# Performance work log

Measured on AMD Instinct MI355X. Metric: run time of the kernel, lower is better.

Reference implementation:

```python
import jax, jax.numpy as jnp
import numpy as np
from jax import lax

B, H, W = 2, 960, 1280
K = 1024            # max_keypoints
P = 256             # num_pairs (BAD descriptor dim)
NUM_SCALES = 3
DIFF_ITERS = 3
KAPPA = 0.05
TAU = 0.2           # explicit FED step size (stable < 0.25)
DET_THRESHOLD = 0.001
AKAZE_NMS = 5       # detector-internal NMS window
NMS_WIN = 2 * 3 + 1 # pipeline NMS window (nms_radius=3)
ORI_PATCH = 15
ORI_SIGMA = 2.5
SINK_ITERS = 20
EPSILON = 1.0
UNUSED_SCORE = 1.0
MAX_RADIUS = 5

def _conv(x, k):
    return lax.conv_general_dilated(x, k, (1, 1), 'SAME', dimension_numbers=('NCHW', 'OIHW', 'NCHW'))

_sob = np.array([[-1., 0., 1.], [-2., 0., 2.], [-1., 0., 1.]], np.float32) / 8.0
KX = jnp.asarray(_sob)[None, None]
KY = jnp.asarray(_sob.T)[None, None]
_d2 = np.array([[0., 0., 0.], [1., -2., 1.], [0., 0., 0.]], np.float32)
KXX = jnp.asarray(_d2)[None, None]
KYY = jnp.asarray(_d2.T)[None, None]

# Gaussian weighting kernel for orientation estimation
_c = np.arange(ORI_PATCH, dtype=np.float32) - (ORI_PATCH - 1) / 2.0
_gy, _gx = np.meshgrid(_c, _c, indexing='ij')
_g = np.exp(-(_gx ** 2 + _gy ** 2) / (2.0 * ORI_SIGMA ** 2))
GK = jnp.asarray((_g / _g.sum()).astype(np.float32))[None, None]

# Box-average kernel bank: one normalized box filter per radius 0..MAX_RADIUS
_bc = np.arange(-MAX_RADIUS, MAX_RADIUS + 1, dtype=np.float32)
_by, _bx = np.meshgrid(_bc, _bc, indexing='ij')
_rv = np.arange(MAX_RADIUS + 1, dtype=np.float32)[:, None, None]
_bm = ((np.abs(_by) <= _rv) & (np.abs(_bx) <= _rv)).astype(np.float32)
BOX_BANK = jnp.asarray((_bm / (2.0 * _rv + 1.0) ** 2)[:, None])  # [R+1,1,11,11]

def _shifts(a):
    p = jnp.pad(a, ((0, 0), (0, 0), (1, 1), (1, 1)), mode='edge')
    return p[:, :, :-2, 1:-1], p[:, :, 2:, 1:-1], p[:, :, 1:-1, :-2], p[:, :, 1:-1, 2:]

def _fed_step(L):
    # One explicit Perona-Malik (FED) nonlinear diffusion step
    Lx = _conv(L, KX); Ly = _conv(L, KY)
    g = 1.0 / (1.0 + (Lx * Lx + Ly * Ly) / (KAPPA * KAPPA))
    Ln, Ls, Lw, Le = _shifts(L)
    gn, gs, gw, ge = _shifts(g)
    flux = 0.5 * ((g + gn) * (Ln - L) + (g + gs) * (Ls - L) + (g + gw) * (Lw - L) + (g + ge) * (Le - L))
    return L + TAU * flux

def _maxpool(s, win):
    return lax.reduce_window(s, -jnp.inf, lax.max, (1, win, win), (1, 1, 1), 'SAME')

def _akaze(img):
    # Multi-scale FED diffusion -> Hessian determinant response + orientation map
    L = img
    resp = jnp.zeros((B, H, W), img.dtype)
    for _s in range(NUM_SCALES):
        for _i in range(DIFF_ITERS):
            L = _fed_step(L)
        Lxx = _conv(L, KXX); Lyy = _conv(L, KYY); Lxy = _conv(_conv(L, KX), KY)
        resp = jnp.maximum(resp, (Lxx * Lyy - Lxy * Lxy)[:, 0])
    resp = jnp.where(resp > DET_THRESHOLD, resp, 0.0)
    resp = resp * (resp >= _maxpool(resp, AKAZE_NMS) - 1e-7).astype(resp.dtype)
    gxs = _conv(_conv(img, KX), GK)[:, 0]
    gys = _conv(_conv(img, KY), GK)[:, 0]
    theta = jnp.arctan2(gys, gxs)  # [B,H,W]
    return resp, theta

def _select(resp):
    # Pipeline-level maxpool NMS + top-K selection, pad invalid with (-1,-1)
    mask = (resp >= _maxpool(resp, NMS_WIN) - 1e-7).astype(resp.dtype)
    s = resp * mask
    s = jnp.where(s > 0.0, s, 0.0)
    tk, idx = lax.top_k(s.reshape(B, -1), K)
    y = (idx // W).astype(jnp.float32)
    x = (idx % W).astype(jnp.float32)
    valid = (tk > 0.0).astype(jnp.float32)
    kpts = jnp.where(valid[..., None] > 0.5, jnp.stack([y, x], -1), -1.0)
    return kpts, tk * valid, valid

def _bad(img, kpts, theta, valid, offsets, radii, thresholds):
    # Orientation-aware BAD: box-averaged intensity differences at rotated pair offsets
    bank = _conv(img, BOX_BANK)  # [B,R+1,H,W]
    yc = jnp.clip(kpts[..., 0], 0.0, H - 1.0)
    xc = jnp.clip(kpts[..., 1], 0.0, W - 1.0)
    yi = jnp.round(yc).astype(jnp.int32); xi = jnp.round(xc).astype(jnp.int32)
    th = jax.vmap(lambda m, a, b: m[a, b])(theta, yi, xi)  # [B,K] nearest-sampled orientation
    c = jnp.cos(th)[..., None]; s = jnp.sin(th)[..., None]
    ox1, oy1, ox2, oy2 = offsets[:, 0], offsets[:, 1], offsets[:, 2], offsets[:, 3]
    px1 = xc[..., None] + c * ox1 - s * oy1
    py1 = yc[..., None] + s * ox1 + c * oy1
    px2 = xc[..., None] + c * ox2 - s * oy2
    py2 = yc[..., None] + s * ox2 + c * oy2
    rb = jnp.broadcast_to(radii[None, :], (K, P))
    def samp(px, py):
        xi_ = jnp.clip(jnp.round(px), 0, W - 1).astype(jnp.int32)
        yi_ = jnp.clip(jnp.round(py), 0, H - 1).astype(jnp.int32)
        return jax.vmap(lambda bk, a, b: bk[rb, a, b])(bank, yi_, xi_)  # [B,K,P]
    v = (samp(px1, py1) - samp(px2, py2)) - thresholds[None, None, :]
    v = v * valid[..., None]
    n = jnp.linalg.norm(v, axis=-1, keepdims=True)
    return v / (n + 1e-8)

def _sinkhorn(d1, d2):
    sq1 = jnp.sum(d1 * d1, -1); sq2 = jnp.sum(d2 * d2, -1)
    dist2 = sq1[:, :, None] + sq2[:, None, :] - 2.0 * jnp.einsum('bip,bjp->bij', d1, d2)
    dist = jnp.sqrt(jnp.maximum(dist2, 0.0) + 1e-12)
    Z = jnp.full((B, K + 1, K + 1), UNUSED_SCORE, d1.dtype)
    Z = Z.at[:, :K, :K].set(-dist) / EPSILON
    norm = -jnp.log(2.0 * K)
    log_mu = jnp.concatenate([jnp.zeros(K, Z.dtype), jnp.log(float(K)) * jnp.ones(1, Z.dtype)]) + norm
    log_nu = log_mu
    def body(carry, _):
        u, v = carry
        u = log_mu[None] - jax.nn.logsumexp(Z + v[:, None, :], axis=2)
        v = log_nu[None] - jax.nn.logsumexp(Z + u[:, :, None], axis=1)
        return (u, v), None
    (u, v), _ = lax.scan(body, (jnp.zeros((B, K + 1), Z.dtype), jnp.zeros((B, K + 1), Z.dtype)), None, length=SINK_ITERS)
    return jnp.exp(Z + u[:, :, None] + v[:, None, :] - norm)  # [B,K+1,K+1]

def _forward(img1, img2, offsets, thresholds, radii):
    r1, t1 = _akaze(img1)
    r2, t2 = _akaze(img2)
    k1, s1, v1 = _select(r1)
    k2, s2, v2 = _select(r2)
    d1 = _bad(img1, k1, t1, v1, offsets, radii, thresholds)
    d2 = _bad(img2, k2, t2, v2, offsets, radii, thresholds)
    probs = _sinkhorn(d1, d2)
    return k1, k2, probs

def setup_inputs():
    key = jax.random.key(0)
    k1, k2, k3, k4, k5 = jax.random.split(key, 5)
    img1 = jax.random.uniform(k1, (B, 1, H, W), jnp.float32)
    img2 = jax.random.uniform(k2, (B, 1, H, W), jnp.float32)
    offsets = jax.random.uniform(k3, (P, 4), jnp.float32, -16.0, 16.0)  # box_params - 16
    thresholds = 0.05 * jax.random.normal(k5, (P,), jnp.float32)
    radii = jax.random.randint(k4, (P,), 0, MAX_RADIUS + 1, jnp.int32)
    return {'img1': img1, 'img2': img2, 'offsets': offsets, 'thresholds': thresholds, 'radii': radii}

def reference(img1, img2, offsets, thresholds, radii):
    return _forward(img1, img2, offsets, thresholds, radii)
```

## Files before the change

### kernel.cpp

```cpp
#include <hip/hip_runtime.h>
#include <hip/hip_fp16.h>
#include <math.h>

typedef unsigned long long u64;
typedef unsigned int u32;

#define Hh 960
#define Ww 1280
#define Bb 2
#define Kk 1024
#define Pp 256
#define KP1 1025
#define NSEG 4
#define LISTCAP 131072
#define PR 28
#define PS 57
#define ZLD 1040
#define CANDCAP 8192
static const size_t ZB = (size_t)KP1*ZLD;

static const size_t HWp = (size_t)Hh * Ww;
static const size_t PLn = HWp * Bb;

#define TAUf 0.2f
#define NMS_EPS 1e-7f
#define DET_T 0.001f
#define NORMV (-7.6246189861593985f)
#define LOGKV (6.9314718055994531f)

__constant__ float WR[6] = {1.0f, 1.0f/9.0f, 1.0f/25.0f, 1.0f/49.0f, 1.0f/81.0f, 1.0f/121.0f};

__device__ __forceinline__ int imin(int a,int b){return a<b?a:b;}
__device__ __forceinline__ int imax(int a,int b){return a>b?a:b;}

__global__ __launch_bounds__(256) void fed_step(const float* __restrict__ src, float* __restrict__ dst){
  __shared__ float Lt[36][37];
  __shared__ float Gt[34][35];
  const int bx = blockIdx.x*32, by = blockIdx.y*32, b = blockIdx.z;
  const float* S = src + (size_t)b*HWp;
  float* D = dst + (size_t)b*HWp;
  const int t = threadIdx.y*32 + threadIdx.x;
  for (int i=t;i<36*36;i+=256){
    int ly=i/36, lx=i-ly*36;
    int gy=by+ly-2, gx=bx+lx-2;
    Lt[ly][lx] = (gy>=0 && gy<Hh && gx>=0 && gx<Ww) ? S[(size_t)gy*Ww+gx] : 0.0f;
  }
  __syncthreads();
  const float k2 = (float)(0.05*0.05);
  for (int i=t;i<34*34;i+=256){
    int ly=i/34, lx=i-ly*34;
    int Ly=ly+1, Lx=lx+1;
    float sx = (-Lt[Ly-1][Lx-1]+Lt[Ly-1][Lx+1]
                -2.0f*Lt[Ly][Lx-1]+2.0f*Lt[Ly][Lx+1]
                -Lt[Ly+1][Lx-1]+Lt[Ly+1][Lx+1])*0.125f;
    float sy = (-Lt[Ly-1][Lx-1]-2.0f*Lt[Ly-1][Lx]-Lt[Ly-1][Lx+1]
                +Lt[Ly+1][Lx-1]+2.0f*Lt[Ly+1][Lx]+Lt[Ly+1][Lx+1])*0.125f;
    Gt[ly][lx] = 1.0f/(1.0f + (sx*sx+sy*sy)/k2);
  }
  __syncthreads();
  for (int r=0;r<4;++r){
    int oy=threadIdx.y + r*8, ox=threadIdx.x;
    int gy=by+oy, gx=bx+ox;
    if (gy>=Hh || gx>=Ww) continue;
    int gyn=imax(gy-1,0), gys=imin(gy+1,Hh-1), gxw=imax(gx-1,0), gxe=imin(gx+1,Ww-1);
    float Lc=Lt[oy+2][ox+2];
    float Ln=Lt[gyn-by+2][ox+2];
    float Ls=Lt[gys-by+2][ox+2];
    float Lw=Lt[oy+2][gxw-bx+2];
    float Le=Lt[oy+2][gxe-bx+2];
    float gc=Gt[oy+1][ox+1];
    float gn=Gt[gyn-by+1][ox+1];
    float gs=Gt[gys-by+1][ox+1];
    float gw=Gt[oy+1][gxw-bx+1];
    float ge=Gt[oy+1][gxe-bx+1];
    float flux = 0.5f*((gc+gn)*(Ln-Lc) + (gc+gs)*(Ls-Lc) + (gc+gw)*(Lw-Lc) + (gc+ge)*(Le-Lc));
    D[(size_t)gy*Ww+gx] = Lc + TAUf*flux;
  }
}

__global__ __launch_bounds__(256) void response_kernel(const float* __restrict__ src, float* __restrict__ resp, int first){
  __shared__ float Lt[36][37];
  __shared__ float Sx[34][35];
  const int bx = blockIdx.x*32, by = blockIdx.y*32, b = blockIdx.z;
  const float* S = src + (size_t)b*HWp;
  float* R = resp + (size_t)b*HWp;
  const int t = threadIdx.y*32 + threadIdx.x;
  for (int i=t;i<36*36;i+=256){
    int ly=i/36, lx=i-ly*36;
    int gy=by+ly-2, gx=bx+lx-2;
    Lt[ly][lx] = (gy>=0 && gy<Hh && gx>=0 && gx<Ww) ? S[(size_t)gy*Ww+gx] : 0.0f;
  }
  __syncthreads();
  for (int i=t;i<34*34;i+=256){
    int ly=i/34, lx=i-ly*34;
    int gy=by+ly-1, gx=bx+lx-1;
    float v=0.0f;
    if (gy>=0 && gy<Hh && gx>=0 && gx<Ww){
      int Ly=ly+1, Lx=lx+1;
      v = (-Lt[Ly-1][Lx-1]+Lt[Ly-1][Lx+1]
           -2.0f*Lt[Ly][Lx-1]+2.0f*Lt[Ly][Lx+1]
           -Lt[Ly+1][Lx-1]+Lt[Ly+1][Lx+1])*0.125f;
    }
    Sx[ly][lx]=v;
  }
  __syncthreads();
  for (int r=0;r<4;++r){
    int oy=threadIdx.y + r*8, ox=threadIdx.x;
    int gy=by+oy, gx=bx+ox;
    if (gy>=Hh || gx>=Ww) continue;
    int Ly=oy+2, Lx=ox+2;
    float Lxx = Lt[Ly][Lx-1]-2.0f*Lt[Ly][Lx]+Lt[Ly][Lx+1];
    float Lyy = Lt[Ly-1][Lx]-2.0f*Lt[Ly][Lx]+Lt[Ly+1][Lx];
    int Sy=oy+1, Sxi=ox+1;
    float Lxy = (-Sx[Sy-1][Sxi-1]-2.0f*Sx[Sy-1][Sxi]-Sx[Sy-1][Sxi+1]
                 +Sx[Sy+1][Sxi-1]+2.0f*Sx[Sy+1][Sxi]+Sx[Sy+1][Sxi+1])*0.125f;
    float det = Lxx*Lyy - Lxy*Lxy;
    size_t id=(size_t)gy*Ww+gx;
    R[id] = first ? fmaxf(det,0.0f) : fmaxf(R[id], det);
  }
}

__global__ __launch_bounds__(256) void detect_compact(const float* __restrict__ resp,
                                                      u64* __restrict__ lists,
                                                      int* __restrict__ cnt, int segbase){
  const int TS=42;
  __shared__ float Tt[TS][TS+1];
  __shared__ float H5[TS][40];
  __shared__ float Ss[38][39];
  __shared__ u64 keys[1024];
  __shared__ int lcnt, gbase;
  const int bx = blockIdx.x*32, by = blockIdx.y*32, b = blockIdx.z;
  const float* S = resp + (size_t)b*HWp;
  const int t = threadIdx.y*32 + threadIdx.x;
  if (t==0) lcnt=0;
  for (int i=t;i<TS*TS;i+=256){
    int ly=i/TS, lx=i-ly*TS;
    int gy=by+ly-5, gx=bx+lx-5;
    float v = (gy>=0 && gy<Hh && gx>=0 && gx<Ww) ? S[(size_t)gy*Ww+gx] : 0.0f;
    Tt[ly][lx] = (v>DET_T) ? v : 0.0f;
  }
  __syncthreads();
  for (int i=t;i<42*38;i+=256){
    int y=i/38, x=i-(i/38)*38;
    float m=Tt[y][x];
    m=fmaxf(m,Tt[y][x+1]); m=fmaxf(m,Tt[y][x+2]);
    m=fmaxf(m,Tt[y][x+3]); m=fmaxf(m,Tt[y][x+4]);
    H5[y][x]=m;
  }
  __syncthreads();
  for (int i=t;i<38*38;i+=256){
    int y=i/38, x=i-(i/38)*38;
    float m=H5[y][x];
    m=fmaxf(m,H5[y+1][x]); m=fmaxf(m,H5[y+2][x]);
    m=fmaxf(m,H5[y+3][x]); m=fmaxf(m,H5[y+4][x]);
    float c=Tt[y+2][x+2];
    Ss[y][x]=(c>=m-NMS_EPS)?c:0.0f;
  }
  __syncthreads();
  const int seg=segbase+b;
  for (int r=0;r<4;++r){
    int oy=threadIdx.y + r*8, ox=threadIdx.x;
    int gy=by+oy, gx=bx+ox;
    bool pos=false; u64 key=0;
    if (gy<Hh && gx<Ww){
      float v=Ss[oy+3][ox+3];
      if (v>0.0f){
        float m=0.0f;
        #pragma unroll
        for(int dy=0;dy<7;dy++)
          #pragma unroll
          for(int dx=0;dx<7;dx++)
            m=fmaxf(m,Ss[oy+dy][ox+dx]);
        if (v>=m-NMS_EPS){
          u32 idx=(u32)(gy*Ww+gx);
          key=((u64)__float_as_uint(v)<<32)|(u64)(0xFFFFFFFFu-idx);
          pos=true;
        }
      }
    }
    u64 mask=__ballot(pos);
    if (mask){
      int lane=t&63;
      int leader=__ffsll((long long)mask)-1;
      int base=0;
      if (lane==leader) base=atomicAdd(&lcnt,__popcll(mask));
      base=__shfl(base,leader);
      if (pos){
        int rk=__popcll(mask & ((1ULL<<lane)-1ULL));
        keys[base+rk]=key;
      }
    }
  }
  __syncthreads();
  if (t==0 && lcnt>0) gbase=atomicAdd(&cnt[seg*64], lcnt);
  __syncthreads();
  int n=lcnt;
  for (int i=t;i<n;i+=256){
    int p=gbase+i;
    if (p<LISTCAP) lists[(size_t)seg*LISTCAP+p]=keys[i];
  }
}

__global__ __launch_bounds__(256) void topk_hist16(const u64* __restrict__ lists, const int* __restrict__ cnt,
                                                   u32* __restrict__ h16){
  int seg=blockIdx.y;
  int n=imin(cnt[seg*64],LISTCAP);
  const u64* L=lists+(size_t)seg*LISTCAP;
  u32* H=h16+(size_t)seg*65536;
  for(int i=blockIdx.x*256+threadIdx.x;i<n;i+=gridDim.x*256){
    u32 b=(u32)(L[i]>>48);
    atomicAdd(&H[b],1u);
  }
}

__global__ __launch_bounds__(1024) void topk_decide16(const u32* __restrict__ h16, const int* __restrict__ cnt,
                                                      int* __restrict__ b16o, int* __restrict__ krem16,
                                                      int* __restrict__ takeAll, u64* __restrict__ Tf){
  int seg=blockIdx.x, tid=threadIdx.x;
  __shared__ u32 sc[1024];
  const u32* H=h16+(size_t)seg*65536;
  int n=imin(cnt[seg*64],LISTCAP);
  if(n<=Kk){
    if(tid==0){ takeAll[seg]=1; Tf[seg]=1ULL; b16o[seg]=-1; }
    return;
  }
  u32 csum=0;
  u32 hl[  64];
  #pragma unroll 8
  for(int j=0;j<64;j++){ hl[j]=H[tid*64+j]; csum+=hl[j]; }
  sc[tid]=csum;
  __syncthreads();
  for(int off=1;off<1024;off<<=1){
    u32 v=(tid+off<1024)?sc[tid+off]:0u;
    __syncthreads();
    sc[tid]+=v;
    __syncthreads();
  }
  u32 nxt=(tid<1023)?sc[tid+1]:0u;
  if(sc[tid]>=(u32)Kk && nxt<(u32)Kk){
    u32 run=nxt;
    for(int j=63;j>=0;j--){
      u32 c=hl[j];
      run+=c;
      if(run>=(u32)Kk){
        b16o[seg]=tid*64+j;
        krem16[seg]=Kk-(int)(run-c);
        takeAll[seg]=0;
        break;
      }
    }
  }
}

__global__ __launch_bounds__(256) void topk_compact(const u64* __restrict__ lists, const int* __restrict__ cnt,
                                                    const int* __restrict__ b16o, const int* __restrict__ takeAll,
                                                    u64* __restrict__ candbuf, int* __restrict__ candcnt){
  int seg=blockIdx.y;
  if(takeAll[seg]) return;
  int n=imin(cnt[seg*64],LISTCAP);
  const u64* L=lists+(size_t)seg*LISTCAP;
  u32 b16=(u32)b16o[seg];
  for(int i0=blockIdx.x*256;i0<n;i0+=gridDim.x*256){
    int i=i0+threadIdx.x;
    bool sel=false; u64 k=0;
    if(i<n){ k=L[i]; sel=((u32)(k>>48)==b16); }
    u64 mask=__ballot(sel);
    if(mask){
      int lane=threadIdx.x&63;
      int leader=__ffsll((long long)mask)-1;
      int base=0;
      if(lane==leader) base=atomicAdd(&candcnt[seg*64],__popcll(mask));
      base=__shfl(base,leader);
      if(sel){
        int p=base+__popcll(mask & ((1ULL<<lane)-1ULL));
        if(p<CANDCAP) candbuf[(size_t)seg*CANDCAP+p]=k;
      }
    }
  }
}

__global__ __launch_bounds__(1024) void topk_finish(const u64* __restrict__ lists, const int* __restrict__ cnt,
                                                    const u64* __restrict__ candbuf, const int* __restrict__ candcnt,
                                                    const int* __restrict__ b16o, const int* __restrict__ krem16,
                                                    const int* __restrict__ takeAll, u64* __restrict__ Tf){
  int seg=blockIdx.x, tid=threadIdx.x;
  if(takeAll[seg]) return;
  __shared__ u64 cands[CANDCAP];
  __shared__ u32 h[256], scan[256];
  __shared__ int bsel;
  int cc=candcnt[seg*64];
  u64 pfx=((u64)(u32)b16o[seg])<<48;
  int kr=krem16[seg];
  if(cc<=CANDCAP){
    for(int i=tid;i<cc;i+=1024) cands[i]=candbuf[(size_t)seg*CANDCAP+i];
    __syncthreads();
    for(int rd=0;rd<6;rd++){
      int shift=40-8*rd;
      u64 maskHi=~0ULL<<(shift+8);
      if(tid<256) h[tid]=0;
      __syncthreads();
      for(int i=tid;i<cc;i+=1024){
        u64 k=cands[i];
        if((k&maskHi)==pfx) atomicAdd(&h[(int)((k>>shift)&255ULL)],1u);
      }
      __syncthreads();
      if(tid<256) scan[tid]=h[tid];
      __syncthreads();
      for(int off=1;off<256;off<<=1){
        u32 v=0;
        if(tid<256 && tid+off<256) v=scan[tid+off];
        __syncthreads();
        if(tid<256) scan[tid]+=v;
        __syncthreads();
      }
      if(tid<256){
        bool ge=(scan[tid]>=(u32)kr);
        bool geN=(tid<255)?(scan[tid+1]>=(u32)kr):false;
        if(ge && !geN) bsel=tid;
      }
      __syncthreads();
      int b=bsel;
      int acc=(b<255)?(int)scan[b+1]:0;
      pfx |= ((u64)(u32)b)<<shift;
      kr -= acc;
      __syncthreads();
    }
  } else {
    int n=imin(cnt[seg*64],LISTCAP);
    const u64* L=lists+(size_t)seg*LISTCAP;
    for(int rd=0;rd<6;rd++){
      int shift=40-8*rd;
      u64 maskHi=~0ULL<<(shift+8);
      if(tid<256) h[tid]=0;
      __syncthreads();
      for(int i=tid;i<n;i+=1024){
        u64 k=L[i];
        if((k&maskHi)==pfx) atomicAdd(&h[(int)((k>>shift)&255ULL)],1u);
      }
      __syncthreads();
      if(tid<256) scan[tid]=h[tid];
      __syncthreads();
      for(int off=1;off<256;off<<=1){
        u32 v=0;
        if(tid<256 && tid+off<256) v=scan[tid+off];
        __syncthreads();
        if(tid<256) scan[tid]+=v;
        __syncthreads();
      }
      if(tid<256){
        bool ge=(scan[tid]>=(u32)kr);
        bool geN=(tid<255)?(scan[tid+1]>=(u32)kr):false;
        if(ge && !geN) bsel=tid;
      }
      __syncthreads();
      int b=bsel;
      int acc=(b<255)?(int)scan[b+1]:0;
      pfx |= ((u64)(u32)b)<<shift;
      kr -= acc;
      __syncthreads();
    }
  }
  if(tid==0) Tf[seg]=pfx;
}

__global__ __launch_bounds__(256) void topk_gather(const u64* __restrict__ lists, const int* __restrict__ cnt,
                                                   const u64* __restrict__ Tf, u64* __restrict__ selbuf,
                                                   int* __restrict__ selcnt){
  int seg=blockIdx.y;
  int n=imin(cnt[seg*64],LISTCAP);
  u64 T=Tf[seg];
  const u64* L=lists+(size_t)seg*LISTCAP;
  for(int i0=blockIdx.x*256;i0<n;i0+=gridDim.x*256){
    int i=i0+threadIdx.x;
    bool sel=false; u64 k=0;
    if(i<n){ k=L[i]; sel=(k>=T); }
    u64 mask=__ballot(sel);
    if(mask){
      int lane=threadIdx.x&63;
      int leader=__ffsll((long long)mask)-1;
      int base=0;
      if(lane==leader) base=atomicAdd(&selcnt[seg*64],__popcll(mask));
      base=__shfl(base,leader);
      if(sel){
        int p=base+__popcll(mask & ((1ULL<<lane)-1ULL));
        if(p<Kk) selbuf[(size_t)seg*Kk+p]=k;
      }
    }
  }
}

__global__ __launch_bounds__(1024) void finalize_kernel(const u64* __restrict__ selbuf, const int* __restrict__ selcnt,
                                int* __restrict__ kyi, int* __restrict__ kxi, float* __restrict__ kval,
                                float* __restrict__ outp){
  int seg=blockIdx.x, tid=threadIdx.x;
  __shared__ u64 a[1024];
  int n=selcnt[seg*64]; if(n>Kk)n=Kk;
  a[tid]=(tid<n)?selbuf[(size_t)seg*Kk+tid]:0ULL;
  __syncthreads();
  for(int k=2;k<=1024;k<<=1){
    for(int j=k>>1;j>0;j>>=1){
      int ixj=tid^j;
      if(ixj>tid){
        u64 x=a[tid], y=a[ixj];
        bool desc=((tid&k)==0);
        if(desc ? (x<y) : (x>y)){ a[tid]=y; a[ixj]=x; }
      }
      __syncthreads();
    }
  }
  u64 key=a[tid];
  bool val=(key!=0ULL);
  u32 idx=0xFFFFFFFFu-(u32)(key&0xFFFFFFFFULL);
  int y= val ? (int)(idx/Ww) : 0;
  int x= val ? (int)(idx%Ww) : 0;
  int mi=seg*Kk+tid;
  kyi[mi]=y; kxi[mi]=x; kval[mi]= val?1.0f:0.0f;
  int imi=seg>>1, bb=seg&1;
  float* ko=outp + (size_t)imi*(Bb*Kk*2) + ((size_t)bb*Kk+tid)*2;
  ko[0]= val ? (float)y : -1.0f;
  ko[1]= val ? (float)x : -1.0f;
}

__global__ void init_weights(float* wn){
  if(threadIdx.x==0 && blockIdx.x==0){
    double w[15]; double S=0.0;
    for(int i=0;i<15;i++){ double c=(double)i-7.0; w[i]=exp(-(c*c)/(2.0*2.5*2.5)); S+=w[i]; }
    for(int i=0;i<15;i++) wn[i]=(float)(w[i]/S);
  }
}

__device__ __forceinline__ float ldz(const float* __restrict__ img,int y,int x){
  return (y>=0&&y<Hh&&x>=0&&x<Ww)?img[(size_t)y*Ww+x]:0.0f;
}

__global__ __launch_bounds__(64) void orient_kernel(const float* __restrict__ img1, const float* __restrict__ img2,
                              const int* __restrict__ kyi, const int* __restrict__ kxi,
                              const float* __restrict__ wn, float* __restrict__ kth){
  int seg=blockIdx.y, ki=blockIdx.x, lane=threadIdx.x;
  __shared__ float w15[15];
  if(lane<15) w15[lane]=wn[lane];
  __syncthreads();
  const float* img=(seg<2?img1:img2)+(size_t)(seg&1)*HWp;
  int mi=seg*Kk+ki;
  int yc=kyi[mi], xc=kxi[mi];
  float ax=0.0f, ay=0.0f;
  for(int tp=lane;tp<225;tp+=64){
    int du=tp/15-7, dv=tp-(tp/15)*15-7;
    int yy=yc+du, xx=xc+dv;
    if(yy<0||yy>=Hh||xx<0||xx>=Ww) continue;
    float p00=ldz(img,yy-1,xx-1), p01=ldz(img,yy-1,xx), p02=ldz(img,yy-1,xx+1);
    float p10=ldz(img,yy,xx-1),                          p12=ldz(img,yy,xx+1);
    float p20=ldz(img,yy+1,xx-1), p21=ldz(img,yy+1,xx), p22=ldz(img,yy+1,xx+1);
    float sx=(-p00+p02-2.0f*p10+2.0f*p12-p20+p22)*0.125f;
    float sy=(-p00-2.0f*p01-p02+p20+2.0f*p21+p22)*0.125f;
    float wgt=w15[du+7]*w15[dv+7];
    ax=fmaf(wgt,sx,ax); ay=fmaf(wgt,sy,ay);
  }
  for(int o=32;o;o>>=1){ ax+=__shfl_down(ax,o); ay+=__shfl_down(ay,o); }
  if(lane==0) kth[mi]=atan2f(ay,ax);
}

__global__ __launch_bounds__(256) void bad_kernel(const float* __restrict__ img1, const float* __restrict__ img2,
                           const float* __restrict__ offs, const float* __restrict__ thrv,
                           const int* __restrict__ rad,
                           const int* __restrict__ kyi, const int* __restrict__ kxi,
                           const float* __restrict__ kval, const float* __restrict__ kth,
                           float* __restrict__ d1, float* __restrict__ d2,
                           float* __restrict__ sq1, float* __restrict__ sq2){
  __shared__ float sat[PS+1][PS+2];
  __shared__ float sm[4];
  __shared__ float nsh;
  int seg=blockIdx.y, ki=blockIdx.x, p=threadIdx.x;
  const float* img=(seg<2?img1:img2)+(size_t)(seg&1)*HWp;
  int mi=seg*Kk+ki;
  int yci=kyi[mi], xci=kxi[mi];
  for (int i=p;i<PS+1;i+=256){ sat[0][i]=0.0f; sat[i][0]=0.0f; }
  if (p==0) sat[0][PS]=0.0f;
  for (int i=p;i<PS*PS;i+=256){
    int ly=i/PS, lx=i-ly*PS;
    int gy=yci-PR+ly, gx=xci-PR+lx;
    sat[ly+1][lx+1]=(gy>=0&&gy<Hh&&gx>=0&&gx<Ww)?img[(size_t)gy*Ww+gx]:0.0f;
  }
  __syncthreads();
  if (p<PS){
    float run=0.0f;
    for(int x=1;x<=PS;x++){ run+=sat[p+1][x]; sat[p+1][x]=run; }
  }
  __syncthreads();
  if (p<PS){
    float run=0.0f;
    for(int y=1;y<=PS;y++){ run+=sat[y][p+1]; sat[y][p+1]=run; }
  }
  __syncthreads();
  float yc=(float)yci, xc=(float)xci;
  float th=kth[mi];
  float c=cosf(th), s=sinf(th);
  float ox1=offs[p*4+0], oy1=offs[p*4+1], ox2=offs[p*4+2], oy2=offs[p*4+3];
  int r=rad[p];
  float w=WR[r];
  float px1=xc+c*ox1-s*oy1, py1=yc+s*ox1+c*oy1;
  float px2=xc+c*ox2-s*oy2, py2=yc+s*ox2+c*oy2;
  auto boxl=[&](float px,float py,int r_)->float{
    float rx=rintf(px), ry=rintf(py);
    int xi=(int)fminf(fmaxf(rx,0.0f),(float)(Ww-1));
    int yi=(int)fminf(fmaxf(ry,0.0f),(float)(Hh-1));
    int lx=xi-(xci-PR), ly=yi-(yci-PR);
    int y2=ly+r_+1, y1=ly-r_, x2=lx+r_+1, x1=lx-r_;
    return sat[y2][x2]-sat[y1][x2]-sat[y2][x1]+sat[y1][x1];
  };
  float s1=boxl(px1,py1,r)*w;
  float s2=boxl(px2,py2,r)*w;
  float v=(s1-s2-thrv[p])*kval[mi];
  float t=v*v;
  for(int o=32;o;o>>=1) t+=__shfl_down(t,o);
  if((p&63)==0) sm[p>>6]=t;
  __syncthreads();
  if(p==0) nsh=sqrtf(sm[0]+sm[1]+sm[2]+sm[3]);
  __syncthreads();
  float dv=v/(nsh+1e-8f);
  float* dd=(seg<2?d1:d2);
  dd[((size_t)(seg&1)*Kk+ki)*Pp+p]=dv;
  float t2=dv*dv;
  for(int o=32;o;o>>=1) t2+=__shfl_down(t2,o);
  __syncthreads();
  if((p&63)==0) sm[p>>6]=t2;
  __syncthreads();
  if(p==0){ float* sq=(seg<2?sq1:sq2); sq[(size_t)(seg&1)*Kk+ki]=sm[0]+sm[1]+sm[2]+sm[3]; }
}

__global__ __launch_bounds__(256) void dist_kernel(const float* __restrict__ d1, const float* __restrict__ d2,
                            const float* __restrict__ sq1, const float* __restrict__ sq2,
                            float* __restrict__ Zm, float* __restrict__ Zt){
  int b=blockIdx.z;
  int i0=blockIdx.y*64, j0=blockIdx.x*64;
  int tid=threadIdx.x;
  int tx=tid&15, ty=tid>>4;
  __shared__ float Ast[64][68], Bst[64][68];
  const float* D1=d1+(size_t)b*Kk*Pp;
  const float* D2=d2+(size_t)b*Kk*Pp;
  float acc[4][4]={};
  for(int p0=0;p0<Pp;p0+=64){
    for(int i=tid;i<64*16;i+=256){
      int row=i>>4, c4=(i&15)<<2;
      float4 va=*reinterpret_cast<const float4*>(&D1[(size_t)(i0+row)*Pp+p0+c4]);
      float4 vb=*reinterpret_cast<const float4*>(&D2[(size_t)(j0+row)*Pp+p0+c4]);
      Ast[c4+0][row]=va.x; Ast[c4+1][row]=va.y; Ast[c4+2][row]=va.z; Ast[c4+3][row]=va.w;
      Bst[c4+0][row]=vb.x; Bst[c4+1][row]=vb.y; Bst[c4+2][row]=vb.z; Bst[c4+3][row]=vb.w;
    }
    __syncthreads();
    #pragma unroll 8
    for(int kk=0;kk<64;++kk){
      float4 av=*reinterpret_cast<const float4*>(&Ast[kk][ty*4]);
      float4 bv=*reinterpret_cast<const float4*>(&Bst[kk][tx*4]);
      acc[0][0]=fmaf(av.x,bv.x,acc[0][0]); acc[0][1]=fmaf(av.x,bv.y,acc[0][1]);
      acc[0][2]=fmaf(av.x,bv.z,acc[0][2]); acc[0][3]=fmaf(av.x,bv.w,acc[0][3]);
      acc[1][0]=fmaf(av.y,bv.x,acc[1][0]); acc[1][1]=fmaf(av.y,bv.y,acc[1][1]);
      acc[1][2]=fmaf(av.y,bv.z,acc[1][2]); acc[1][3]=fmaf(av.y,bv.w,acc[1][3]);
      acc[2][0]=fmaf(av.z,bv.x,acc[2][0]); acc[2][1]=fmaf(av.z,bv.y,acc[2][1]);
      acc[2][2]=fmaf(av.z,bv.z,acc[2][2]); acc[2][3]=fmaf(av.z,bv.w,acc[2][3]);
      acc[3][0]=fmaf(av.w,bv.x,acc[3][0]); acc[3][1]=fmaf(av.w,bv.y,acc[3][1]);
      acc[3][2]=fmaf(av.w,bv.z,acc[3][2]); acc[3][3]=fmaf(av.w,bv.w,acc[3][3]);
    }
    __syncthreads();
  }
  int gi=i0+ty*4, gj=j0+tx*4;
  float si[4], sj[4];
  #pragma unroll
  for(int i=0;i<4;i++){ si[i]=sq1[b*Kk+gi+i]; sj[i]=sq2[b*Kk+gj+i]; }
  #pragma unroll
  for(int i=0;i<4;i++){
    #pragma unroll
    for(int j=0;j<4;j++){
      float dd=si[i]+sj[j]-2.0f*acc[i][j];
      float dist=sqrtf(fmaxf(dd,0.0f)+1e-12f);
      Zm[(size_t)b*ZB+(size_t)(gi+i)*ZLD+(gj+j)]=-dist;
      Zt[(size_t)b*ZB+(size_t)(gj+j)*ZLD+(gi+i)]=-dist;
    }
  }
}

__global__ void zborder_kernel(float* __restrict__ Zm, float* __restrict__ Zt){
  int i=blockIdx.x*256+threadIdx.x;
  if(i>=Bb*KP1) return;
  int b=i/KP1, j=i-(i/KP1)*KP1;
  size_t base=(size_t)b*ZB;
  Zm[base+(size_t)j*ZLD+Kk]=1.0f;
  Zm[base+(size_t)Kk*ZLD+j]=1.0f;
  Zt[base+(size_t)j*ZLD+Kk]=1.0f;
  Zt[base+(size_t)Kk*ZLD+j]=1.0f;
  for(int c=KP1;c<ZLD;c++){
    Zm[base+(size_t)j*ZLD+c]=-1.0e30f;
    Zt[base+(size_t)j*ZLD+c]=-1.0e30f;
  }
}

__global__ void expz_kernel(const float* __restrict__ Zm, const float* __restrict__ Zt,
                            __half* __restrict__ Em, __half* __restrict__ Et){
  size_t q=(size_t)blockIdx.x*256+threadIdx.x;
  const size_t tot4=(size_t)Bb*ZB/4;
  if(q>=2*tot4) return;
  const float* src=(q<tot4)?Zm:Zt;
  __half* dst=(q<tot4)?Em:Et;
  size_t j=(q<tot4)?q:q-tot4;
  float4 z=reinterpret_cast<const float4*>(src)[j];
  __half2 a=__floats2half2_rn(expf(z.x),expf(z.y));
  __half2 b=__floats2half2_rn(expf(z.z),expf(z.w));
  reinterpret_cast<__half2*>(dst)[2*j]=a;
  reinterpret_cast<__half2*>(dst)[2*j+1]=b;
}

__global__ void init_euv(float* __restrict__ euv, float* __restrict__ evv){
  int i=blockIdx.x*256+threadIdx.x;
  if(i>=Bb*ZLD) return;
  int j=i-(i/ZLD)*ZLD;
  evv[i]=(j<KP1)?1.0f:0.0f;
  euv[i]=0.0f;
}

struct H4{ __half2 a, b; };
__global__ __launch_bounds__(256) void sink_gemv(const __half* __restrict__ E,
        const float* __restrict__ evin, float* __restrict__ euout, float* __restrict__ uout){
  int row=blockIdx.x*4+(threadIdx.x>>6);
  if(row>=Bb*KP1) return;
  int b=row/KP1, i=row-b*KP1;
  int lane=threadIdx.x&63;
  const H4* e4=reinterpret_cast<const H4*>(E+((size_t)b*KP1+i)*ZLD);
  const float4* v4=reinterpret_cast<const float4*>(evin+(size_t)b*ZLD);
  float s=0.0f;
  for(int j=lane;j<ZLD/4;j+=64){
    H4 e=e4[j]; float4 v=v4[j];
    float2 ea=__half22float2(e.a), eb=__half22float2(e.b);
    s=fmaf(ea.x,v.x,s); s=fmaf(ea.y,v.y,s);
    s=fmaf(eb.x,v.z,s); s=fmaf(eb.y,v.w,s);
  }
  for(int o=32;o;o>>=1) s+=__shfl_down(s,o);
  if(lane==0){
    float lm,elm;
    if(i<Kk){ lm=NORMV; elm=4.8828125e-4f; }
    else    { lm=LOGKV+NORMV; elm=0.5f; }
    euout[(size_t)b*ZLD+i]=elm/s;
    uout [(size_t)b*ZLD+i]=lm-logf(s);
  }
}

__global__ void probs_kernel(const float* __restrict__ Zm, const float* __restrict__ uu,
                             const float* __restrict__ vv, float* __restrict__ outp){
  size_t i=(size_t)blockIdx.x*256+threadIdx.x;
  const size_t tot=(size_t)Bb*KP1*KP1;
  if(i>=tot) return;
  size_t b=i/((size_t)KP1*KP1);
  size_t rem=i-b*(size_t)KP1*KP1;
  int rr=(int)(rem/KP1), cc=(int)(rem-(size_t)(rem/KP1)*KP1);
  outp[i]=expf(Zm[b*ZB+(size_t)rr*ZLD+cc]+uu[b*ZLD+rr]+vv[b*ZLD+cc]-NORMV);
}

extern "C" void kernel_launch(void* const* d_in, const int* in_sizes, int n_in,
                              void* d_out, int out_size, void* d_ws, size_t ws_size,
                              hipStream_t stream) {
  (void)in_sizes; (void)n_in; (void)out_size;
  const float* img1=(const float*)d_in[0];
  const float* img2=(const float*)d_in[1];
  const float* offs=(const float*)d_in[2];
  const float* thrv=(const float*)d_in[3];
  const int*   rad =(const int*)d_in[4];
  float* out=(float*)d_out;

  const bool batched = ws_size >= ((size_t)80<<20);
  const int NP = batched ? 4 : 2;
  const size_t PB = HWp*(size_t)NP*4;

  char* wp=(char*)d_ws;
  auto carve=[&](size_t bytes)->char*{ char* p=wp; wp += (bytes+255)&~(size_t)255; return p; };
  float* r0  =(float*)carve(PB);
  float* r1  =(float*)carve(PB);
  float* resp=(float*)carve(PB);
  u64*  lists=(u64*)carve((size_t)NSEG*LISTCAP*8);
  char* stateblk = carve(8192);
  int* cnt     =(int*)(stateblk);
  int* selcnt  =(int*)(stateblk+1024);
  int* b16o    =(int*)(stateblk+2048);
  int* krem16  =(int*)(stateblk+2112);
  int* takeAll =(int*)(stateblk+2176);
  u64* Tf      =(u64*)(stateblk+2240);
  int* candcnt =(int*)(stateblk+4096);
  u32* h16     =(u32*)carve((size_t)NSEG*65536*4);
  u64* candbuf =(u64*)carve((size_t)NSEG*CANDCAP*8);
  u64* selbuf  =(u64*)carve((size_t)NSEG*Kk*8);
  int* kyi     =(int*)carve((size_t)NSEG*Kk*4);
  int* kxi     =(int*)carve((size_t)NSEG*Kk*4);
  float* kval  =(float*)carve((size_t)NSEG*Kk*4);
  float* kth   =(float*)carve((size_t)NSEG*Kk*4);
  float* d1    =(float*)carve((size_t)Bb*Kk*Pp*4);
  float* d2    =(float*)carve((size_t)Bb*Kk*Pp*4);
  float* sq1   =(float*)carve((size_t)Bb*Kk*4);
  float* sq2   =(float*)carve((size_t)Bb*Kk*4);
  float* uvec  =(float*)carve((size_t)Bb*ZLD*4);
  float* vvec  =(float*)carve((size_t)Bb*ZLD*4);
  float* euvec =(float*)carve((size_t)Bb*ZLD*4);
  float* evvec =(float*)carve((size_t)Bb*ZLD*4);
  float* wn    =(float*)carve(64);

  const size_t EBYTES = ((size_t)Bb*ZB*2 + 255)&~(size_t)255;
  __half* Em=(__half*)resp;
  __half* Et=(__half*)((char*)resp + EBYTES);

  hipMemsetAsync(stateblk, 0, 8192, stream);
  hipMemsetAsync(h16, 0, (size_t)NSEG*65536*4, stream);
  init_weights<<<1,32,0,stream>>>(wn);

  dim3 TB(32,8);
  if (batched){
    dim3 TG(Ww/32, Hh/32, 4);
    hipMemcpyAsync(r0,       img1, PLn*4, hipMemcpyDeviceToDevice, stream);
    hipMemcpyAsync(r0+2*HWp, img2, PLn*4, hipMemcpyDeviceToDevice, stream);
    float* cur=r0; float* oth=r1;
    for(int st=1; st<=9; ++st){
      fed_step<<<TG,TB,0,stream>>>(cur, oth);
      float* tp=cur; cur=oth; oth=tp;
      if(st%3==0) response_kernel<<<TG,TB,0,stream>>>(cur, resp, st==3);
    }
    detect_compact<<<TG,TB,0,stream>>>(resp, lists, cnt, 0);
  } else {
    dim3 TG(Ww/32, Hh/32, Bb);
    for(int im=0; im<2; ++im){
      const float* srcimg = (im==0)? img1 : img2;
      hipMemcpyAsync(r0, srcimg, PLn*4, hipMemcpyDeviceToDevice, stream);
      float* cur=r0; float* oth=r1;
      for(int st=1; st<=9; ++st){
        fed_step<<<TG,TB,0,stream>>>(cur, oth);
        float* tp=cur; cur=oth; oth=tp;
        if(st%3==0) response_kernel<<<TG,TB,0,stream>>>(cur, resp, st==3);
      }
      detect_compact<<<TG,TB,0,stream>>>(resp, lists, cnt, im*2);
    }
  }

  topk_hist16 <<<dim3(32,NSEG),dim3(256),0,stream>>>(lists, cnt, h16);
  topk_decide16<<<dim3(NSEG),dim3(1024),0,stream>>>(h16, cnt, b16o, krem16, takeAll, Tf);
  topk_compact<<<dim3(32,NSEG),dim3(256),0,stream>>>(lists, cnt, b16o, takeAll, candbuf, candcnt);
  topk_finish <<<dim3(NSEG),dim3(1024),0,stream>>>(lists, cnt, candbuf, candcnt, b16o, krem16, takeAll, Tf);
  topk_gather <<<dim3(32,NSEG),dim3(256),0,stream>>>(lists, cnt, Tf, selbuf, selcnt);
  finalize_kernel<<<NSEG,1024,0,stream>>>(selbuf, selcnt, kyi, kxi, kval, out);
  orient_kernel<<<dim3(Kk,NSEG),dim3(64),0,stream>>>(img1, img2, kyi, kxi, wn, kth);
  bad_kernel<<<dim3(Kk,NSEG),dim3(256),0,stream>>>(img1, img2, offs, thrv, rad,
                                                   kyi, kxi, kval, kth, d1, d2, sq1, sq2);

  float* Zm=r0; float* Zt=r1;
  dist_kernel<<<dim3(16,16,Bb),dim3(256),0,stream>>>(d1,d2,sq1,sq2,Zm,Zt);
  zborder_kernel<<<dim3((Bb*KP1+255)/256),dim3(256),0,stream>>>(Zm,Zt);
  {
    size_t tot4=(size_t)Bb*ZB/4;
    expz_kernel<<<dim3((u32)((2*tot4+255)/256)),dim3(256),0,stream>>>(Zm,Zt,Em,Et);
  }
  init_euv<<<dim3((Bb*ZLD+255)/256),dim3(256),0,stream>>>(euvec,evvec);
  for(int it=0; it<20; ++it){
    sink_gemv<<<dim3((Bb*KP1+3)/4),dim3(256),0,stream>>>(Em, evvec, euvec, uvec);
    sink_gemv<<<dim3((Bb*KP1+3)/4),dim3(256),0,stream>>>(Et, euvec, evvec, vvec);
  }
  size_t tot=(size_t)Bb*KP1*KP1;
  probs_kernel<<<dim3((u32)((tot+255)/256)),dim3(256),0,stream>>>(Zm, uvec, vvec, out + (size_t)2*Bb*Kk*2);
}
```

Before: 628.7 us.

## Fuse FED step with Hessian response, fold orientation into BAD kernel

Every third diffusion step now runs a combined kernel that computes the FED update on a haloed tile, keeps the result in shared memory, and evaluates the Hessian determinant response directly, so the separate response pass no longer re-reads the diffused image. The orientation kernel is removed and its Sobel-weighted sums are computed inside the BAD kernel from the patch already staged in shared memory. Detector NMS merges the separable 5x5 max into one direct 25-tap loop, dropping an intermediate buffer and a barrier. In exchange the fused kernel redundantly computes a wider halo and needs more shared memory per block, which may lower occupancy.

```diff
diff --git a/kernel.cpp b/kernel.cpp
--- a/kernel.cpp
+++ b/kernel.cpp
@@ -78,45 +78,76 @@
   }
 }
 
-__global__ __launch_bounds__(256) void response_kernel(const float* __restrict__ src, float* __restrict__ resp, int first){
-  __shared__ float Lt[36][37];
-  __shared__ float Sx[34][35];
-  const int bx = blockIdx.x*32, by = blockIdx.y*32, b = blockIdx.z;
-  const float* S = src + (size_t)b*HWp;
-  float* R = resp + (size_t)b*HWp;
-  const int t = threadIdx.y*32 + threadIdx.x;
-  for (int i=t;i<36*36;i+=256){
-    int ly=i/36, lx=i-ly*36;
-    int gy=by+ly-2, gx=bx+lx-2;
-    Lt[ly][lx] = (gy>=0 && gy<Hh && gx>=0 && gx<Ww) ? S[(size_t)gy*Ww+gx] : 0.0f;
-  }
-  __syncthreads();
-  for (int i=t;i<34*34;i+=256){
-    int ly=i/34, lx=i-ly*34;
-    int gy=by+ly-1, gx=bx+lx-1;
+__global__ __launch_bounds__(256) void fed_step_resp(const float* __restrict__ src, float* __restrict__ dstL,
+                                                     float* __restrict__ resp, int first){
+  __shared__ float Lt[40][41];
+  __shared__ float Gt[38][39];
+  __shared__ float Lp[36][37];
+  const int bx=blockIdx.x*32, by=blockIdx.y*32, b=blockIdx.z;
+  const int gx0=bx-4, gy0=by-4;
+  const float* S=src+(size_t)b*HWp;
+  float* DL=dstL+(size_t)b*HWp;
+  float* R=resp+(size_t)b*HWp;
+  const int t=threadIdx.y*32+threadIdx.x;
+  const float k2=(float)(0.05*0.05);
+  for(int i=t;i<40*40;i+=256){
+    int ly=i/40, lx=i-(i/40)*40;
+    int gy=gy0+ly, gx=gx0+lx;
+    Lt[ly][lx]=(gy>=0&&gy<Hh&&gx>=0&&gx<Ww)?S[(size_t)gy*Ww+gx]:0.0f;
+  }
+  __syncthreads();
+  for(int i=t;i<38*38;i+=256){
+    int y=i/38+1, x=i-(i/38)*38+1;
+    float sx=(-Lt[y-1][x-1]+Lt[y-1][x+1]
+              -2.0f*Lt[y][x-1]+2.0f*Lt[y][x+1]
+              -Lt[y+1][x-1]+Lt[y+1][x+1])*0.125f;
+    float sy=(-Lt[y-1][x-1]-2.0f*Lt[y-1][x]-Lt[y-1][x+1]
+              +Lt[y+1][x-1]+2.0f*Lt[y+1][x]+Lt[y+1][x+1])*0.125f;
+    Gt[y-1][x-1]=1.0f/(1.0f+(sx*sx+sy*sy)/k2);
+  }
+  __syncthreads();
+  for(int i=t;i<36*36;i+=256){
+    int y=i/36+2, x=i-(i/36)*36+2;
+    int gy=gy0+y, gx=gx0+x;
     float v=0.0f;
-    if (gy>=0 && gy<Hh && gx>=0 && gx<Ww){
-      int Ly=ly+1, Lx=lx+1;
-      v = (-Lt[Ly-1][Lx-1]+Lt[Ly-1][Lx+1]
-           -2.0f*Lt[Ly][Lx-1]+2.0f*Lt[Ly][Lx+1]
-           -Lt[Ly+1][Lx-1]+Lt[Ly+1][Lx+1])*0.125f;
-    }
-    Sx[ly][lx]=v;
-  }
-  __syncthreads();
-  for (int r=0;r<4;++r){
-    int oy=threadIdx.y + r*8, ox=threadIdx.x;
-    int gy=by+oy, gx=bx+ox;
-    if (gy>=Hh || gx>=Ww) continue;
-    int Ly=oy+2, Lx=ox+2;
-    float Lxx = Lt[Ly][Lx-1]-2.0f*Lt[Ly][Lx]+Lt[Ly][Lx+1];
-    float Lyy = Lt[Ly-1][Lx]-2.0f*Lt[Ly][Lx]+Lt[Ly+1][Lx];
-    int Sy=oy+1, Sxi=ox+1;
-    float Lxy = (-Sx[Sy-1][Sxi-1]-2.0f*Sx[Sy-1][Sxi]-Sx[Sy-1][Sxi+1]
-                 +Sx[Sy+1][Sxi-1]+2.0f*Sx[Sy+1][Sxi]+Sx[Sy+1][Sxi+1])*0.125f;
-    float det = Lxx*Lyy - Lxy*Lxy;
-    size_t id=(size_t)gy*Ww+gx;
-    R[id] = first ? fmaxf(det,0.0f) : fmaxf(R[id], det);
+    if(gy>=0&&gy<Hh&&gx>=0&&gx<Ww){
+      int yn=imax(gy-1,0)-gy0, ys=imin(gy+1,Hh-1)-gy0;
+      int xw=imax(gx-1,0)-gx0, xe=imin(gx+1,Ww-1)-gx0;
+      float Lc=Lt[y][x];
+      float Ln=Lt[yn][x], Ls=Lt[ys][x], Lw=Lt[y][xw], Le=Lt[y][xe];
+      float gc=Gt[y-1][x-1], gn=Gt[yn-1][x-1], gs=Gt[ys-1][x-1], gw=Gt[y-1][xw-1], ge=Gt[y-1][xe-1];
+      float flux=0.5f*((gc+gn)*(Ln-Lc)+(gc+gs)*(Ls-Lc)+(gc+gw)*(Lw-Lc)+(gc+ge)*(Le-Lc));
+      v=Lc+TAUf*flux;
+    }
+    Lp[y-2][x-2]=v;
+  }
+  __syncthreads();
+  for(int i=t;i<32*32;i+=256){
+    int oy=i>>5, ox=i&31;
+    DL[(size_t)(by+oy)*Ww+(bx+ox)]=Lp[oy+2][ox+2];
+  }
+  for(int i=t;i<34*34;i+=256){
+    int y=i/34+1, x=i-(i/34)*34+1;
+    int gy=gy0+2+y, gx=gx0+2+x;
+    float v=0.0f;
+    if(gy>=0&&gy<Hh&&gx>=0&&gx<Ww){
+      v=(-Lp[y-1][x-1]+Lp[y-1][x+1]
+         -2.0f*Lp[y][x-1]+2.0f*Lp[y][x+1]
+         -Lp[y+1][x-1]+Lp[y+1][x+1])*0.125f;
+    }
+    Gt[y-1][x-1]=v;
+  }
+  __syncthreads();
+  for(int i=t;i<32*32;i+=256){
+    int oy=i>>5, ox=i&31;
+    int y=oy+2, x=ox+2;
+    float Lxx=Lp[y][x-1]-2.0f*Lp[y][x]+Lp[y][x+1];
+    float Lyy=Lp[y-1][x]-2.0f*Lp[y][x]+Lp[y+1][x];
+    float Lxy=(-Gt[y-2][x-2]-2.0f*Gt[y-2][x-1]-Gt[y-2][x]
+               +Gt[y][x-2]+2.0f*Gt[y][x-1]+Gt[y][x])*0.125f;
+    float det=Lxx*Lyy-Lxy*Lxy;
+    size_t id=(size_t)(by+oy)*Ww+(bx+ox);
+    R[id]=first?fmaxf(det,0.0f):fmaxf(R[id],det);
   }
 }
 
@@ -125,7 +156,6 @@
                                                       int* __restrict__ cnt, int segbase){
   const int TS=42;
   __shared__ float Tt[TS][TS+1];
-  __shared__ float H5[TS][40];
   __shared__ float Ss[38][39];
   __shared__ u64 keys[1024];
   __shared__ int lcnt, gbase;
@@ -140,21 +170,17 @@
     Tt[ly][lx] = (v>DET_T) ? v : 0.0f;
   }
   __syncthreads();
-  for (int i=t;i<42*38;i+=256){
-    int y=i/38, x=i-(i/38)*38;
-    float m=Tt[y][x];
-    m=fmaxf(m,Tt[y][x+1]); m=fmaxf(m,Tt[y][x+2]);
-    m=fmaxf(m,Tt[y][x+3]); m=fmaxf(m,Tt[y][x+4]);
-    H5[y][x]=m;
-  }
-  __syncthreads();
   for (int i=t;i<38*38;i+=256){
-    int y=i/38, x=i-(i/38)*38;
-    float m=H5[y][x];
-    m=fmaxf(m,H5[y+1][x]); m=fmaxf(m,H5[y+2][x]);
-    m=fmaxf(m,H5[y+3][x]); m=fmaxf(m,H5[y+4][x]);
-    float c=Tt[y+2][x+2];
-    Ss[y][x]=(c>=m-NMS_EPS)?c:0.0f;
+    int ly=i/38, lx=i-ly*38;
+    int ty=ly+2, tx=lx+2;
+    float m=0.0f;
+    #pragma unroll
+    for(int dy=-2;dy<=2;dy++)
+      #pragma unroll
+      for(int dx=-2;dx<=2;dx++)
+        m=fmaxf(m,Tt[ty+dy][tx+dx]);
+    float c=Tt[ty][tx];
+    Ss[ly][lx]=(c>=m-NMS_EPS)?c:0.0f;
   }
   __syncthreads();
   const int seg=segbase+b;
@@ -225,7 +251,7 @@
     return;
   }
   u32 csum=0;
-  u32 hl[  64];
+  u32 hl[64];
   #pragma unroll 8
   for(int j=0;j<64;j++){ hl[j]=H[tid*64+j]; csum+=hl[j]; }
   sc[tid]=csum;
@@ -429,51 +455,22 @@
   }
 }
 
-__device__ __forceinline__ float ldz(const float* __restrict__ img,int y,int x){
-  return (y>=0&&y<Hh&&x>=0&&x<Ww)?img[(size_t)y*Ww+x]:0.0f;
-}
-
-__global__ __launch_bounds__(64) void orient_kernel(const float* __restrict__ img1, const float* __restrict__ img2,
-                              const int* __restrict__ kyi, const int* __restrict__ kxi,
-                              const float* __restrict__ wn, float* __restrict__ kth){
-  int seg=blockIdx.y, ki=blockIdx.x, lane=threadIdx.x;
-  __shared__ float w15[15];
-  if(lane<15) w15[lane]=wn[lane];
-  __syncthreads();
-  const float* img=(seg<2?img1:img2)+(size_t)(seg&1)*HWp;
-  int mi=seg*Kk+ki;
-  int yc=kyi[mi], xc=kxi[mi];
-  float ax=0.0f, ay=0.0f;
-  for(int tp=lane;tp<225;tp+=64){
-    int du=tp/15-7, dv=tp-(tp/15)*15-7;
-    int yy=yc+du, xx=xc+dv;
-    if(yy<0||yy>=Hh||xx<0||xx>=Ww) continue;
-    float p00=ldz(img,yy-1,xx-1), p01=ldz(img,yy-1,xx), p02=ldz(img,yy-1,xx+1);
-    float p10=ldz(img,yy,xx-1),                          p12=ldz(img,yy,xx+1);
-    float p20=ldz(img,yy+1,xx-1), p21=ldz(img,yy+1,xx), p22=ldz(img,yy+1,xx+1);
-    float sx=(-p00+p02-2.0f*p10+2.0f*p12-p20+p22)*0.125f;
-    float sy=(-p00-2.0f*p01-p02+p20+2.0f*p21+p22)*0.125f;
-    float wgt=w15[du+7]*w15[dv+7];
-    ax=fmaf(wgt,sx,ax); ay=fmaf(wgt,sy,ay);
-  }
-  for(int o=32;o;o>>=1){ ax+=__shfl_down(ax,o); ay+=__shfl_down(ay,o); }
-  if(lane==0) kth[mi]=atan2f(ay,ax);
-}
-
 __global__ __launch_bounds__(256) void bad_kernel(const float* __restrict__ img1, const float* __restrict__ img2,
                            const float* __restrict__ offs, const float* __restrict__ thrv,
-                           const int* __restrict__ rad,
+                           const int* __restrict__ rad, const float* __restrict__ wn,
                            const int* __restrict__ kyi, const int* __restrict__ kxi,
-                           const float* __restrict__ kval, const float* __restrict__ kth,
+                           const float* __restrict__ kval,
                            float* __restrict__ d1, float* __restrict__ d2,
                            float* __restrict__ sq1, float* __restrict__ sq2){
   __shared__ float sat[PS+1][PS+2];
-  __shared__ float sm[4];
-  __shared__ float nsh;
+  __shared__ float sm[4], smx[4], smy[4];
+  __shared__ float w15s[15];
+  __shared__ float nsh, thsh;
   int seg=blockIdx.y, ki=blockIdx.x, p=threadIdx.x;
   const float* img=(seg<2?img1:img2)+(size_t)(seg&1)*HWp;
   int mi=seg*Kk+ki;
   int yci=kyi[mi], xci=kxi[mi];
+  if(p<15) w15s[p]=wn[p];
   for (int i=p;i<PS+1;i+=256){ sat[0][i]=0.0f; sat[i][0]=0.0f; }
   if (p==0) sat[0][PS]=0.0f;
   for (int i=p;i<PS*PS;i+=256){
@@ -482,6 +479,28 @@
     sat[ly+1][lx+1]=(gy>=0&&gy<Hh&&gx>=0&&gx<Ww)?img[(size_t)gy*Ww+gx]:0.0f;
   }
   __syncthreads();
+  {
+    float ax=0.0f, ay=0.0f;
+    if(p<225){
+      int du=p/15-7, dv=p-(p/15)*15-7;
+      int yy=yci+du, xx=xci+dv;
+      if(yy>=0&&yy<Hh&&xx>=0&&xx<Ww){
+        int ly=du+PR+1, lx=dv+PR+1;
+        float p00=sat[ly-1][lx-1], p01=sat[ly-1][lx], p02=sat[ly-1][lx+1];
+        float p10=sat[ly][lx-1],                       p12=sat[ly][lx+1];
+        float p20=sat[ly+1][lx-1], p21=sat[ly+1][lx], p22=sat[ly+1][lx+1];
+        float sx=(-p00+p02-2.0f*p10+2.0f*p12-p20+p22)*0.125f;
+        float sy=(-p00-2.0f*p01-p02+p20+2.0f*p21+p22)*0.125f;
+        float wgt=w15s[du+7]*w15s[dv+7];
+        ax=wgt*sx; ay=wgt*sy;
+      }
+    }
+    for(int o=32;o;o>>=1){ ax+=__shfl_down(ax,o); ay+=__shfl_down(ay,o); }
+    if((p&63)==0){ smx[p>>6]=ax; smy[p>>6]=ay; }
+    __syncthreads();
+    if(p==0) thsh=atan2f(smy[0]+smy[1]+smy[2]+smy[3], smx[0]+smx[1]+smx[2]+smx[3]);
+  }
+  __syncthreads();
   if (p<PS){
     float run=0.0f;
     for(int x=1;x<=PS;x++){ run+=sat[p+1][x]; sat[p+1][x]=run; }
@@ -493,7 +512,7 @@
   }
   __syncthreads();
   float yc=(float)yci, xc=(float)xci;
-  float th=kth[mi];
+  float th=thsh;
   float c=cosf(th), s=sinf(th);
   float ox1=offs[p*4+0], oy1=offs[p*4+1], ox2=offs[p*4+2], oy2=offs[p*4+3];
   int r=rad[p];
@@ -689,7 +708,6 @@
   int* kyi     =(int*)carve((size_t)NSEG*Kk*4);
   int* kxi     =(int*)carve((size_t)NSEG*Kk*4);
   float* kval  =(float*)carve((size_t)NSEG*Kk*4);
-  float* kth   =(float*)carve((size_t)NSEG*Kk*4);
   float* d1    =(float*)carve((size_t)Bb*Kk*Pp*4);
   float* d2    =(float*)carve((size_t)Bb*Kk*Pp*4);
   float* sq1   =(float*)carve((size_t)Bb*Kk*4);
@@ -715,9 +733,9 @@
     hipMemcpyAsync(r0+2*HWp, img2, PLn*4, hipMemcpyDeviceToDevice, stream);
     float* cur=r0; float* oth=r1;
     for(int st=1; st<=9; ++st){
-      fed_step<<<TG,TB,0,stream>>>(cur, oth);
+      if(st%3==0) fed_step_resp<<<TG,TB,0,stream>>>(cur, oth, resp, st==3);
+      else        fed_step<<<TG,TB,0,stream>>>(cur, oth);
       float* tp=cur; cur=oth; oth=tp;
-      if(st%3==0) response_kernel<<<TG,TB,0,stream>>>(cur, resp, st==3);
     }
     detect_compact<<<TG,TB,0,stream>>>(resp, lists, cnt, 0);
   } else {
@@ -727,9 +745,9 @@
       hipMemcpyAsync(r0, srcimg, PLn*4, hipMemcpyDeviceToDevice, stream);
       float* cur=r0; float* oth=r1;
       for(int st=1; st<=9; ++st){
-        fed_step<<<TG,TB,0,stream>>>(cur, oth);
+        if(st%3==0) fed_step_resp<<<TG,TB,0,stream>>>(cur, oth, resp, st==3);
+        else        fed_step<<<TG,TB,0,stream>>>(cur, oth);
         float* tp=cur; cur=oth; oth=tp;
-        if(st%3==0) response_kernel<<<TG,TB,0,stream>>>(cur, resp, st==3);
       }
       detect_compact<<<TG,TB,0,stream>>>(resp, lists, cnt, im*2);
     }
@@ -741,9 +759,8 @@
   topk_finish <<<dim3(NSEG),dim3(1024),0,stream>>>(lists, cnt, candbuf, candcnt, b16o, krem16, takeAll, Tf);
   topk_gather <<<dim3(32,NSEG),dim3(256),0,stream>>>(lists, cnt, Tf, selbuf, selcnt);
   finalize_kernel<<<NSEG,1024,0,stream>>>(selbuf, selcnt, kyi, kxi, kval, out);
-  orient_kernel<<<dim3(Kk,NSEG),dim3(64),0,stream>>>(img1, img2, kyi, kxi, wn, kth);
-  bad_kernel<<<dim3(Kk,NSEG),dim3(256),0,stream>>>(img1, img2, offs, thrv, rad,
-                                                   kyi, kxi, kval, kth, d1, d2, sq1, sq2);
+  bad_kernel<<<dim3(Kk,NSEG),dim3(256),0,stream>>>(img1, img2, offs, thrv, rad, wn,
+                                                   kyi, kxi, kval, d1, d2, sq1, sq2);
 
   float* Zm=r0; float* Zt=r1;
   dist_kernel<<<dim3(16,16,Bb),dim3(256),0,stream>>>(d1,d2,sq1,sq2,Zm,Zt);
```

Result: faster. 596.1 us (-5.2%).
